# Optimization experiments

Measured on AMD Instinct MI355X. Metric: run time of the kernel, lower is better.

## Reference

```python
import jax, jax.numpy as jnp
import numpy as np

B, L, NS, D, M = 64, 200, 1000, 128, 50


def setup_inputs() -> dict:
    key = jax.random.key(0)
    ks = jax.random.split(key, 12)
    s = np.sqrt(2.0 / D).astype(np.float32)  # kaiming_normal scale for Mk/Mv0
    lw = np.sqrt(1.0 / D).astype(np.float32)
    return {
        "skills": jax.random.randint(ks[0], (B, L), 0, NS),
        "responses": jax.random.randint(ks[1], (B, L), 0, 2),
        "k_emb": jax.random.normal(ks[2], (NS, D), jnp.float32) * 0.02,
        "v_emb": jax.random.normal(ks[3], (2 * NS, D), jnp.float32) * 0.02,
        "Mk": jax.random.normal(ks[4], (M, D), jnp.float32) * s,
        "Mv0": jax.random.normal(ks[5], (M, D), jnp.float32) * s,
        "e_W": jax.random.normal(ks[6], (D, D), jnp.float32) * lw,
        "e_b": jnp.zeros((D,), jnp.float32),
        "a_W": jax.random.normal(ks[7], (D, D), jnp.float32) * lw,
        "a_b": jnp.zeros((D,), jnp.float32),
        "f_W": jax.random.normal(ks[8], (D, 2 * D), jnp.float32) * np.sqrt(1.0 / (2 * D)).astype(np.float32),
        "f_b": jnp.zeros((D,), jnp.float32),
        "p_W": jax.random.normal(ks[9], (1, D), jnp.float32) * lw,
        "p_b": jnp.zeros((1,), jnp.float32),
    }


def _dkvmn_forward(skills, responses, k_emb, v_emb, Mk, Mv0,
                   e_W, e_b, a_W, a_b, f_W, f_b, p_W, p_b):
    masked_r = responses * (responses > -1).astype(responses.dtype)
    x = skills + NS * masked_r                      # [B,L] combined (skill,response) id
    k = k_emb[skills]                               # [B,L,D]
    v = v_emb[x]                                    # [B,L,D]
    w = jax.nn.softmax(jnp.einsum('bld,md->blm', k, Mk), axis=-1)  # [B,L,M]
    e = jax.nn.sigmoid(v @ e_W.T + e_b)             # erase  [B,L,D]
    a = jnp.tanh(v @ a_W.T + a_b)                   # add    [B,L,D]

    def step(Mvt, wea):
        wt, et, at = wea                            # [B,M], [B,D], [B,D]
        u = wt[:, :, None]                          # [B,M,1]
        new = Mvt * (1.0 - u * et[:, None, :]) + u * at[:, None, :]
        return new, Mvt                             # emit PRE-update state (Mv[:, :-1])

    Mv_init = jnp.broadcast_to(Mv0[None], (B, M, D))
    _, Mv_pre = jax.lax.scan(
        step, Mv_init,
        (w.transpose(1, 0, 2), e.transpose(1, 0, 2), a.transpose(1, 0, 2)))
    # Mv_pre: [L,B,M,D]; weighted read of pre-update memory
    read = jnp.einsum('blm,lbmd->bld', w, Mv_pre)   # [B,L,D]
    f = jnp.tanh(jnp.concatenate([read, k], axis=-1) @ f_W.T + f_b)  # [B,L,D]
    p = jax.nn.sigmoid(f @ p_W.T + p_b)[..., 0]     # [B,L] (dropout off: eval)
    return p[:, 1:]                                 # pred, [B,L-1]


def reference(skills, responses, k_emb, v_emb, Mk, Mv0,
              e_W, e_b, a_W, a_b, f_W, f_b, p_W, p_b):
    return _dkvmn_forward(skills, responses, k_emb, v_emb, Mk, Mv0,
                          e_W, e_b, a_W, a_b, f_W, f_b, p_W, p_b)
```

## Files before the change

### kernel.cpp

```cpp
#include <hip/hip_runtime.h>
#include <hip/hip_bf16.h>

#define Bb 64
#define Ll 200
#define NSs 1000
#define Dd 128
#define Mm 50
#define CCk 8
#define TT 25

__device__ __forceinline__ float bcast_lane(float v, int l) {
    return __int_as_float(__builtin_amdgcn_readlane(__float_as_int(v), l));
}

__global__ void __launch_bounds__(256) kern_tab(
        const float* __restrict__ k_emb,
        const float* __restrict__ v_emb,
        const float* __restrict__ Mk,
        const float* __restrict__ e_W, const float* __restrict__ e_b,
        const float* __restrict__ a_W, const float* __restrict__ a_b,
        const float* __restrict__ f_W,
        float* __restrict__ wtab, float* __restrict__ etab,
        float* __restrict__ atab, float* __restrict__ fktab) {
    __shared__ float smem[12672];
    int tid = threadIdx.x;
    int wave = tid >> 6, lane = tid & 63;

    if (blockIdx.x >= 63 && blockIdx.x < 126) {
        int sk0 = (blockIdx.x - 63) * 16;
        float (*mk)[Dd + 4] = (float(*)[Dd + 4])smem;
        float (*kr)[Dd + 4] = (float(*)[Dd + 4])(smem + 6600);
        for (int lin = tid; lin < (Mm * Dd) / 4; lin += 256) {
            float4 f = ((const float4*)Mk)[lin];
            *(float4*)&mk[lin >> 5][(lin & 31) * 4] = f;
        }
        for (int lin = tid; lin < 16 * 32; lin += 256) {
            int r = lin >> 5, c4 = lin & 31;
            int sk = min(sk0 + r, NSs - 1);
            float4 f = ((const float4*)(k_emb + (size_t)sk * Dd))[c4];
            *(float4*)&kr[r][c4 * 4] = f;
        }
        __syncthreads();
        int mmr = (lane < Mm) ? lane : 0;
        float acc[4] = {0.f, 0.f, 0.f, 0.f};
#pragma unroll 2
        for (int q = 0; q < 32; ++q) {
            float4 mkv = *(const float4*)&mk[mmr][q * 4];
#pragma unroll
            for (int i = 0; i < 4; ++i) {
                float4 kv = *(const float4*)&kr[wave * 4 + i][q * 4];
                acc[i] = fmaf(mkv.x, kv.x, acc[i]);
                acc[i] = fmaf(mkv.y, kv.y, acc[i]);
                acc[i] = fmaf(mkv.z, kv.z, acc[i]);
                acc[i] = fmaf(mkv.w, kv.w, acc[i]);
            }
        }
#pragma unroll
        for (int i = 0; i < 4; ++i) {
            float logit = (lane < Mm) ? acc[i] : -1e30f;
            float mx = logit;
            for (int off = 32; off > 0; off >>= 1) mx = fmaxf(mx, __shfl_down(mx, off));
            mx = __shfl(mx, 0);
            float ex = (lane < Mm) ? expf(logit - mx) : 0.f;
            float sm = ex;
            for (int off = 32; off > 0; off >>= 1) sm += __shfl_down(sm, off);
            sm = __shfl(sm, 0);
            int sk = sk0 + wave * 4 + i;
            if (sk < NSs && lane < Mm) wtab[(size_t)sk * Mm + lane] = ex / sm;
        }
        return;
    }

    bool is_fk = (blockIdx.x >= 126);
    int r0 = is_fk ? (blockIdx.x - 126) * 32 : blockIdx.x * 32;
    int rmax = is_fk ? NSs : 2 * NSs;
    const float* src = is_fk ? k_emb : v_emb;

    float (*vt)[Dd + 4] = (float(*)[Dd + 4])smem;
    float (*wt)[Dd + 4] = (float(*)[Dd + 4])(smem + 4224);
#pragma unroll
    for (int i = 0; i < 4; ++i) {
        int lin = i * 256 + tid;
        int r = lin >> 5, c4 = lin & 31;
        int x = min(r0 + r, rmax - 1);
        float4 f = ((const float4*)(src + (size_t)x * Dd))[c4];
        *(float4*)&vt[r][c4 * 4] = f;
    }
    __syncthreads();
    int pg = lane >> 3, og = lane & 7;

    if (is_fk) {
        for (int sub = 0; sub < 2; ++sub) {
#pragma unroll
            for (int i = 0; i < 8; ++i) {
                int lin = i * 64 + lane;
                int r = lin >> 5, c4 = lin & 31;
                int row = wave * 32 + sub * 16 + r;
                float4 f = ((const float4*)(f_W + (size_t)row * (2 * Dd)))[32 + c4];
                *(float4*)&wt[wave * 16 + r][c4 * 4] = f;
            }
            float acc[4][2] = {};
#pragma unroll 2
            for (int q = 0; q < 32; ++q) {
                float4 av[4], bv[2];
#pragma unroll
                for (int i = 0; i < 4; ++i) av[i] = *(const float4*)&vt[pg + 8 * i][q * 4];
#pragma unroll
                for (int j = 0; j < 2; ++j) bv[j] = *(const float4*)&wt[wave * 16 + og + 8 * j][q * 4];
#pragma unroll
                for (int i = 0; i < 4; ++i)
#pragma unroll
                    for (int j = 0; j < 2; ++j) {
                        acc[i][j] = fmaf(av[i].x, bv[j].x, acc[i][j]);
                        acc[i][j] = fmaf(av[i].y, bv[j].y, acc[i][j]);
                        acc[i][j] = fmaf(av[i].z, bv[j].z, acc[i][j]);
                        acc[i][j] = fmaf(av[i].w, bv[j].w, acc[i][j]);
                    }
            }
#pragma unroll
            for (int j = 0; j < 2; ++j) {
                int row = wave * 32 + sub * 16 + og + 8 * j;
#pragma unroll
                for (int i = 0; i < 4; ++i) {
                    int sk = r0 + pg + 8 * i;
                    if (sk < NSs) fktab[(size_t)sk * Dd + row] = acc[i][j];
                }
            }
        }
    } else {
        for (int s = 0; s < 4; ++s) {
            int base_row = wave * 64 + s * 16;
            bool is_e = base_row < 128;
            const float* W = is_e ? e_W : a_W;
            int wrow0 = is_e ? base_row : base_row - 128;
#pragma unroll
            for (int i = 0; i < 8; ++i) {
                int lin = i * 64 + lane;
                int r = lin >> 5, c4 = lin & 31;
                float4 f = ((const float4*)(W + (size_t)(wrow0 + r) * Dd))[c4];
                *(float4*)&wt[wave * 16 + r][c4 * 4] = f;
            }
            float acc[4][2] = {};
#pragma unroll 2
            for (int q = 0; q < 32; ++q) {
                float4 av[4], bv[2];
#pragma unroll
                for (int i = 0; i < 4; ++i) av[i] = *(const float4*)&vt[pg + 8 * i][q * 4];
#pragma unroll
                for (int j = 0; j < 2; ++j) bv[j] = *(const float4*)&wt[wave * 16 + og + 8 * j][q * 4];
#pragma unroll
                for (int i = 0; i < 4; ++i)
#pragma unroll
                    for (int j = 0; j < 2; ++j) {
                        acc[i][j] = fmaf(av[i].x, bv[j].x, acc[i][j]);
                        acc[i][j] = fmaf(av[i].y, bv[j].y, acc[i][j]);
                        acc[i][j] = fmaf(av[i].z, bv[j].z, acc[i][j]);
                        acc[i][j] = fmaf(av[i].w, bv[j].w, acc[i][j]);
                    }
            }
            float* dst = is_e ? etab : atab;
#pragma unroll
            for (int j = 0; j < 2; ++j) {
                int row = wrow0 + og + 8 * j;
                float bias = (is_e ? e_b : a_b)[row];
#pragma unroll
                for (int i = 0; i < 4; ++i) {
                    int x = r0 + pg + 8 * i;
                    if (x < 2 * NSs) {
                        float v = acc[i][j] + bias;
                        dst[(size_t)x * Dd + row] = is_e ? (1.f / (1.f + expf(-v))) : tanhf(v);
                    }
                }
            }
        }
    }
}

#define TB_LOAD(S, tt) do { int _t = (tt);                                   \
    if (_t < TT) {                                                           \
        int _sk = __shfl(skv, _t);                                           \
        int _x  = __shfl(xv, _t);                                            \
        w##S = (lane < Mm) ? wtab[(size_t)_sk * Mm + lane] : 0.f;            \
        e##S = etab[(size_t)_x * Dd + d];                                    \
        a##S = atab[(size_t)_x * Dd + d]; } } while (0)

#define PQ_BODY(S) do {                                                      \
    _Pragma("unroll")                                                        \
    for (int m = 0; m < Mm; ++m) {                                           \
        float wm = bcast_lane(w##S, m);                                      \
        float A  = fmaf(-wm, e##S, 1.f);                                     \
        Q[m] = fmaf(A, Q[m], wm * a##S);                                     \
        P[m] *= A; } } while (0)

#define RD_BODY(S, tt) do {                                                  \
    float acc0 = 0.f, acc1 = 0.f;                                            \
    _Pragma("unroll")                                                        \
    for (int m = 0; m < Mm; m += 2) {                                        \
        float wm0 = bcast_lane(w##S, m);                                     \
        float wm1 = bcast_lane(w##S, m + 1);                                 \
        acc0 = fmaf(wm0, mv[m], acc0);                                       \
        mv[m] = fmaf(wm0, fmaf(-e##S, mv[m], a##S), mv[m]);                  \
        acc1 = fmaf(wm1, mv[m + 1], acc1);                                   \
        mv[m + 1] = fmaf(wm1, fmaf(-e##S, mv[m + 1], a##S), mv[m + 1]);      \
    }                                                                        \
    read_ws[(blBase + (tt)) * Dd + d] = acc0 + acc1;                         \
    } while (0)

__global__ void __launch_bounds__(128) kern_scan_pq(
        const int* __restrict__ skills,
        const int* __restrict__ responses,
        const float* __restrict__ wtab,
        const float* __restrict__ etab,
        const float* __restrict__ atab,
        float* __restrict__ P_ws, float* __restrict__ Q_ws) {
    int b = blockIdx.x / (CCk - 1), c = blockIdx.x % (CCk - 1);
    int d = threadIdx.x;
    int lane = d & 63;
    size_t blBase = (size_t)b * Ll + (size_t)c * TT;

    int skv = 0, xv = 0;
    if (lane < TT) {
        skv = skills[blBase + lane];
        int rr = responses[blBase + lane];
        xv = skv + NSs * ((rr > -1) ? rr : 0);
    }

    float P[Mm], Q[Mm];
#pragma unroll
    for (int m = 0; m < Mm; ++m) { P[m] = 1.f; Q[m] = 0.f; }

    float w0 = 0.f, e0 = 0.f, a0 = 0.f;
    float w1 = 0.f, e1 = 0.f, a1 = 0.f;
    float w2 = 0.f, e2 = 0.f, a2 = 0.f;
    TB_LOAD(0, 0);
    TB_LOAD(1, 1);
    for (int tt = 0; tt < TT; tt += 3) {
        TB_LOAD(2, tt + 2);  PQ_BODY(0);
        if (tt + 1 < TT) { TB_LOAD(0, tt + 3);  PQ_BODY(1); }
        if (tt + 2 < TT) { TB_LOAD(1, tt + 4);  PQ_BODY(2); }
    }
    size_t base = ((size_t)(b * (CCk - 1) + c)) * (Mm * Dd) + d;
#pragma unroll
    for (int m = 0; m < Mm; ++m) {
        P_ws[base + m * Dd] = P[m];
        Q_ws[base + m * Dd] = Q[m];
    }
}

__global__ void __launch_bounds__(128) kern_scan_rd(
        const int* __restrict__ skills,
        const int* __restrict__ responses,
        const float* __restrict__ Mv0,
        const float* __restrict__ wtab,
        const float* __restrict__ etab,
        const float* __restrict__ atab,
        const float* __restrict__ P_ws, const float* __restrict__ Q_ws,
        float* __restrict__ read_ws) {
    int b = blockIdx.x / CCk, c = blockIdx.x % CCk;
    int d = threadIdx.x;
    int lane = d & 63;
    size_t blBase = (size_t)b * Ll + (size_t)c * TT;

    int skv = 0, xv = 0;
    if (lane < TT) {
        skv = skills[blBase + lane];
        int rr = responses[blBase + lane];
        xv = skv + NSs * ((rr > -1) ? rr : 0);
    }

    float mv[Mm];
#pragma unroll
    for (int m = 0; m < Mm; ++m) mv[m] = Mv0[m * Dd + d];
    for (int cc = 0; cc < c; ++cc) {
        size_t base = ((size_t)(b * (CCk - 1) + cc)) * (Mm * Dd) + d;
#pragma unroll
        for (int m = 0; m < Mm; ++m)
            mv[m] = fmaf(P_ws[base + m * Dd], mv[m], Q_ws[base + m * Dd]);
    }

    float w0 = 0.f, e0 = 0.f, a0 = 0.f;
    float w1 = 0.f, e1 = 0.f, a1 = 0.f;
    float w2 = 0.f, e2 = 0.f, a2 = 0.f;
    TB_LOAD(0, 0);
    TB_LOAD(1, 1);
    for (int tt = 0; tt < TT; tt += 3) {
        TB_LOAD(2, tt + 2);  RD_BODY(0, tt);
        if (tt + 1 < TT) { TB_LOAD(0, tt + 3);  RD_BODY(1, tt + 1); }
        if (tt + 2 < TT) { TB_LOAD(1, tt + 4);  RD_BODY(2, tt + 2); }
    }
}

__global__ void __launch_bounds__(256) kern_out(
        const int* __restrict__ skills,
        const float* __restrict__ read_ws,
        const float* __restrict__ fktab,
        const float* __restrict__ f_W, const float* __restrict__ f_b,
        const float* __restrict__ p_W, const float* __restrict__ p_b,
        float* __restrict__ out) {
    __shared__ float ct[32][Dd + 4];
    __shared__ float fkt[32][Dd + 4];
    __shared__ float wt[4][16][Dd + 4];
    __shared__ float pf[32][8];
    int tid = threadIdx.x;
    int blk = blockIdx.x;

#pragma unroll
    for (int i = 0; i < 4; ++i) {
        int lin = i * 256 + tid;
        int r = lin >> 5, c4 = lin & 31;
        int idx = blk * 32 + r;
        int b = idx / (Ll - 1);
        int l = idx % (Ll - 1) + 1;
        int bl = b * Ll + l;
        float4 f = ((const float4*)(read_ws + (size_t)bl * Dd))[c4];
        *(float4*)&ct[r][c4 * 4] = f;
        int sk = skills[bl];
        float4 g = ((const float4*)(fktab + (size_t)sk * Dd))[c4];
        *(float4*)&fkt[r][c4 * 4] = g;
    }
    ((float*)pf)[tid] = 0.f;
    __syncthreads();

    int wave = tid >> 6, lane = tid & 63;
    int pg = lane >> 3, og = lane & 7;

    float ppart[4] = {0.f, 0.f, 0.f, 0.f};
    for (int sub = 0; sub < 2; ++sub) {
        float acc[4][2] = {};
#pragma unroll
        for (int i = 0; i < 8; ++i) {
            int lin = i * 64 + lane;
            int r = lin >> 5, c4 = lin & 31;
            int row = wave * 32 + sub * 16 + r;
            float4 f = ((const float4*)(f_W + (size_t)row * (2 * Dd)))[c4];
            *(float4*)&wt[wave][r][c4 * 4] = f;
        }
#pragma unroll 2
        for (int q = 0; q < 32; ++q) {
            float4 av[4], bv[2];
#pragma unroll
            for (int i = 0; i < 4; ++i) av[i] = *(const float4*)&ct[pg + 8 * i][q * 4];
#pragma unroll
            for (int j = 0; j < 2; ++j) bv[j] = *(const float4*)&wt[wave][og + 8 * j][q * 4];
#pragma unroll
            for (int i = 0; i < 4; ++i)
#pragma unroll
                for (int j = 0; j < 2; ++j) {
                    acc[i][j] = fmaf(av[i].x, bv[j].x, acc[i][j]);
                    acc[i][j] = fmaf(av[i].y, bv[j].y, acc[i][j]);
                    acc[i][j] = fmaf(av[i].z, bv[j].z, acc[i][j]);
                    acc[i][j] = fmaf(av[i].w, bv[j].w, acc[i][j]);
                }
        }
#pragma unroll
        for (int j = 0; j < 2; ++j) {
            int row = wave * 32 + sub * 16 + og + 8 * j;
            float fb = f_b[row];
            float pw = p_W[row];
#pragma unroll
            for (int i = 0; i < 4; ++i) {
                float fkv = fkt[pg + 8 * i][row];
                ppart[i] = fmaf(tanhf(acc[i][j] + fkv + fb), pw, ppart[i]);
            }
        }
    }
#pragma unroll
    for (int i = 0; i < 4; ++i) {
        float v = ppart[i];
        for (int off = 4; off > 0; off >>= 1) v += __shfl_down(v, off, 8);
        if (og == 0) pf[pg + 8 * i][wave] = v;
    }
    __syncthreads();
    if (tid < 32) {
        float s = pf[tid][0] + pf[tid][1] + pf[tid][2] + pf[tid][3] + p_b[0];
        out[blk * 32 + tid] = 1.f / (1.f + expf(-s));
    }
}

extern "C" void kernel_launch(void* const* d_in, const int* in_sizes, int n_in,
                              void* d_out, int out_size, void* d_ws, size_t ws_size,
                              hipStream_t stream) {
    const int*   skills    = (const int*)  d_in[0];
    const int*   responses = (const int*)  d_in[1];
    const float* k_emb     = (const float*)d_in[2];
    const float* v_emb     = (const float*)d_in[3];
    const float* Mk        = (const float*)d_in[4];
    const float* Mv0       = (const float*)d_in[5];
    const float* e_W       = (const float*)d_in[6];
    const float* e_b       = (const float*)d_in[7];
    const float* a_W       = (const float*)d_in[8];
    const float* a_b       = (const float*)d_in[9];
    const float* f_W       = (const float*)d_in[10];
    const float* f_b       = (const float*)d_in[11];
    const float* p_W       = (const float*)d_in[12];
    const float* p_b       = (const float*)d_in[13];
    (void)in_sizes; (void)n_in; (void)out_size; (void)ws_size;

    float* out = (float*)d_out;

    const size_t BLD = (size_t)Bb * Ll * Dd;
    const size_t BMD = (size_t)Bb * Mm * Dd;

    float* ws      = (float*)d_ws;
    float* read_ws = ws;
    float* P_ws    = read_ws + BLD;
    float* Q_ws    = P_ws + (CCk - 1) * BMD;
    float* wtab    = Q_ws + (CCk - 1) * BMD;
    float* etab    = wtab + (size_t)NSs * Mm;
    float* atab    = etab + (size_t)2 * NSs * Dd;
    float* fktab   = atab + (size_t)2 * NSs * Dd;

    kern_tab<<<158, 256, 0, stream>>>(k_emb, v_emb, Mk, e_W, e_b, a_W, a_b, f_W,
                                      wtab, etab, atab, fktab);
    kern_scan_pq<<<Bb * (CCk - 1), 128, 0, stream>>>(skills, responses,
                                                     wtab, etab, atab, P_ws, Q_ws);
    kern_scan_rd<<<Bb * CCk, 128, 0, stream>>>(skills, responses, Mv0,
                                               wtab, etab, atab, P_ws, Q_ws, read_ws);
    kern_out<<<Bb * (Ll - 1) / 32, 256, 0, stream>>>(skills, read_ws, fktab,
                                                     f_W, f_b, p_W, p_b, out);
}
```

Before: 181.3 us.

## Fuse scan read pass with output projection into one kernel

Merges the read-scan kernel and the output MLP kernel so the per-chunk read vectors stay in shared memory instead of round-tripping through a global workspace. Two waves run the scan while the other two stage the f_W tile and key features in parallel, then all four waves compute the projection for the chunk's 25 positions. This removes one launch and the read_ws traffic. In exchange each block reloads the 128x128 weight tile, uses a large shared-memory footprint that may limit occupancy, and wastes lanes on padded positions (25 of 32 rows).

```diff
diff --git a/kernel.cpp b/kernel.cpp
--- a/kernel.cpp
+++ b/kernel.cpp
@@ -203,7 +203,7 @@
         acc1 = fmaf(wm1, mv[m + 1], acc1);                                   \
         mv[m + 1] = fmaf(wm1, fmaf(-e##S, mv[m + 1], a##S), mv[m + 1]);      \
     }                                                                        \
-    read_ws[(blBase + (tt)) * Dd + d] = acc0 + acc1;                         \
+    rt[(tt)][d] = acc0 + acc1;                                               \
     } while (0)
 
 __global__ void __launch_bounds__(128) kern_scan_pq(
@@ -247,7 +247,7 @@
     }
 }
 
-__global__ void __launch_bounds__(128) kern_scan_rd(
+__global__ void __launch_bounds__(256) kern_rd_out(
         const int* __restrict__ skills,
         const int* __restrict__ responses,
         const float* __restrict__ Mv0,
@@ -255,113 +255,100 @@
         const float* __restrict__ etab,
         const float* __restrict__ atab,
         const float* __restrict__ P_ws, const float* __restrict__ Q_ws,
-        float* __restrict__ read_ws) {
-    int b = blockIdx.x / CCk, c = blockIdx.x % CCk;
-    int d = threadIdx.x;
-    int lane = d & 63;
-    size_t blBase = (size_t)b * Ll + (size_t)c * TT;
-
-    int skv = 0, xv = 0;
-    if (lane < TT) {
-        skv = skills[blBase + lane];
-        int rr = responses[blBase + lane];
-        xv = skv + NSs * ((rr > -1) ? rr : 0);
-    }
-
-    float mv[Mm];
-#pragma unroll
-    for (int m = 0; m < Mm; ++m) mv[m] = Mv0[m * Dd + d];
-    for (int cc = 0; cc < c; ++cc) {
-        size_t base = ((size_t)(b * (CCk - 1) + cc)) * (Mm * Dd) + d;
-#pragma unroll
-        for (int m = 0; m < Mm; ++m)
-            mv[m] = fmaf(P_ws[base + m * Dd], mv[m], Q_ws[base + m * Dd]);
-    }
-
-    float w0 = 0.f, e0 = 0.f, a0 = 0.f;
-    float w1 = 0.f, e1 = 0.f, a1 = 0.f;
-    float w2 = 0.f, e2 = 0.f, a2 = 0.f;
-    TB_LOAD(0, 0);
-    TB_LOAD(1, 1);
-    for (int tt = 0; tt < TT; tt += 3) {
-        TB_LOAD(2, tt + 2);  RD_BODY(0, tt);
-        if (tt + 1 < TT) { TB_LOAD(0, tt + 3);  RD_BODY(1, tt + 1); }
-        if (tt + 2 < TT) { TB_LOAD(1, tt + 4);  RD_BODY(2, tt + 2); }
-    }
-}
-
-__global__ void __launch_bounds__(256) kern_out(
-        const int* __restrict__ skills,
-        const float* __restrict__ read_ws,
         const float* __restrict__ fktab,
         const float* __restrict__ f_W, const float* __restrict__ f_b,
         const float* __restrict__ p_W, const float* __restrict__ p_b,
         float* __restrict__ out) {
-    __shared__ float ct[32][Dd + 4];
-    __shared__ float fkt[32][Dd + 4];
-    __shared__ float wt[4][16][Dd + 4];
-    __shared__ float pf[32][8];
+    __shared__ float wtile[Dd][Dd + 4];
+    __shared__ float rt[TT][Dd + 4];
+    __shared__ float fkt[TT][Dd + 4];
+    __shared__ float pf[32][4];
     int tid = threadIdx.x;
-    int blk = blockIdx.x;
-
-#pragma unroll
-    for (int i = 0; i < 4; ++i) {
-        int lin = i * 256 + tid;
-        int r = lin >> 5, c4 = lin & 31;
-        int idx = blk * 32 + r;
-        int b = idx / (Ll - 1);
-        int l = idx % (Ll - 1) + 1;
-        int bl = b * Ll + l;
-        float4 f = ((const float4*)(read_ws + (size_t)bl * Dd))[c4];
-        *(float4*)&ct[r][c4 * 4] = f;
-        int sk = skills[bl];
-        float4 g = ((const float4*)(fktab + (size_t)sk * Dd))[c4];
-        *(float4*)&fkt[r][c4 * 4] = g;
-    }
-    ((float*)pf)[tid] = 0.f;
+    int b = blockIdx.x / CCk, c = blockIdx.x % CCk;
+    size_t blBase = (size_t)b * Ll + (size_t)c * TT;
+
+    if (tid < 128) {
+        int d = tid;
+        int lane = d & 63;
+        int skv = 0, xv = 0;
+        if (lane < TT) {
+            skv = skills[blBase + lane];
+            int rr = responses[blBase + lane];
+            xv = skv + NSs * ((rr > -1) ? rr : 0);
+        }
+        float mv[Mm];
+#pragma unroll
+        for (int m = 0; m < Mm; ++m) mv[m] = Mv0[m * Dd + d];
+        for (int cc = 0; cc < c; ++cc) {
+            size_t base = ((size_t)(b * (CCk - 1) + cc)) * (Mm * Dd) + d;
+#pragma unroll
+            for (int m = 0; m < Mm; ++m)
+                mv[m] = fmaf(P_ws[base + m * Dd], mv[m], Q_ws[base + m * Dd]);
+        }
+        float w0 = 0.f, e0 = 0.f, a0 = 0.f;
+        float w1 = 0.f, e1 = 0.f, a1 = 0.f;
+        float w2 = 0.f, e2 = 0.f, a2 = 0.f;
+        TB_LOAD(0, 0);
+        TB_LOAD(1, 1);
+        for (int tt = 0; tt < TT; tt += 3) {
+            TB_LOAD(2, tt + 2);  RD_BODY(0, tt);
+            if (tt + 1 < TT) { TB_LOAD(0, tt + 3);  RD_BODY(1, tt + 1); }
+            if (tt + 2 < TT) { TB_LOAD(1, tt + 4);  RD_BODY(2, tt + 2); }
+        }
+    } else {
+        int u = tid - 128;
+#pragma unroll
+        for (int i = 0; i < 32; ++i) {
+            int lin = i * 128 + u;
+            int r = lin >> 5, c4 = lin & 31;
+            float4 f = ((const float4*)(f_W + (size_t)r * (2 * Dd)))[c4];
+            *(float4*)&wtile[r][c4 * 4] = f;
+        }
+        for (int lin = u; lin < TT * 32; lin += 128) {
+            int r = lin >> 5, c4 = lin & 31;
+            int sk = skills[blBase + r];
+            float4 f = ((const float4*)(fktab + (size_t)sk * Dd))[c4];
+            *(float4*)&fkt[r][c4 * 4] = f;
+        }
+    }
     __syncthreads();
 
     int wave = tid >> 6, lane = tid & 63;
     int pg = lane >> 3, og = lane & 7;
 
+    float acc[4][4] = {};
+#pragma unroll 2
+    for (int q = 0; q < 32; ++q) {
+        float4 av[4], bv[4];
+#pragma unroll
+        for (int i = 0; i < 4; ++i) {
+            int pos = pg + 8 * i;
+            av[i] = *(const float4*)&rt[(pos < TT) ? pos : 0][q * 4];
+        }
+#pragma unroll
+        for (int j = 0; j < 4; ++j) bv[j] = *(const float4*)&wtile[wave * 32 + og + 8 * j][q * 4];
+#pragma unroll
+        for (int i = 0; i < 4; ++i)
+#pragma unroll
+            for (int j = 0; j < 4; ++j) {
+                acc[i][j] = fmaf(av[i].x, bv[j].x, acc[i][j]);
+                acc[i][j] = fmaf(av[i].y, bv[j].y, acc[i][j]);
+                acc[i][j] = fmaf(av[i].z, bv[j].z, acc[i][j]);
+                acc[i][j] = fmaf(av[i].w, bv[j].w, acc[i][j]);
+            }
+    }
+
     float ppart[4] = {0.f, 0.f, 0.f, 0.f};
-    for (int sub = 0; sub < 2; ++sub) {
-        float acc[4][2] = {};
-#pragma unroll
-        for (int i = 0; i < 8; ++i) {
-            int lin = i * 64 + lane;
-            int r = lin >> 5, c4 = lin & 31;
-            int row = wave * 32 + sub * 16 + r;
-            float4 f = ((const float4*)(f_W + (size_t)row * (2 * Dd)))[c4];
-            *(float4*)&wt[wave][r][c4 * 4] = f;
-        }
-#pragma unroll 2
-        for (int q = 0; q < 32; ++q) {
-            float4 av[4], bv[2];
-#pragma unroll
-            for (int i = 0; i < 4; ++i) av[i] = *(const float4*)&ct[pg + 8 * i][q * 4];
-#pragma unroll
-            for (int j = 0; j < 2; ++j) bv[j] = *(const float4*)&wt[wave][og + 8 * j][q * 4];
-#pragma unroll
-            for (int i = 0; i < 4; ++i)
-#pragma unroll
-                for (int j = 0; j < 2; ++j) {
-                    acc[i][j] = fmaf(av[i].x, bv[j].x, acc[i][j]);
-                    acc[i][j] = fmaf(av[i].y, bv[j].y, acc[i][j]);
-                    acc[i][j] = fmaf(av[i].z, bv[j].z, acc[i][j]);
-                    acc[i][j] = fmaf(av[i].w, bv[j].w, acc[i][j]);
-                }
-        }
-#pragma unroll
-        for (int j = 0; j < 2; ++j) {
-            int row = wave * 32 + sub * 16 + og + 8 * j;
-            float fb = f_b[row];
-            float pw = p_W[row];
-#pragma unroll
-            for (int i = 0; i < 4; ++i) {
-                float fkv = fkt[pg + 8 * i][row];
-                ppart[i] = fmaf(tanhf(acc[i][j] + fkv + fb), pw, ppart[i]);
-            }
+#pragma unroll
+    for (int j = 0; j < 4; ++j) {
+        int row = wave * 32 + og + 8 * j;
+        float fb = f_b[row];
+        float pw = p_W[row];
+#pragma unroll
+        for (int i = 0; i < 4; ++i) {
+            int pos = pg + 8 * i;
+            float fkv = fkt[(pos < TT) ? pos : 0][row];
+            ppart[i] = fmaf(tanhf(acc[i][j] + fkv + fb), pw, ppart[i]);
         }
     }
 #pragma unroll
@@ -371,9 +358,12 @@
         if (og == 0) pf[pg + 8 * i][wave] = v;
     }
     __syncthreads();
-    if (tid < 32) {
-        float s = pf[tid][0] + pf[tid][1] + pf[tid][2] + pf[tid][3] + p_b[0];
-        out[blk * 32 + tid] = 1.f / (1.f + expf(-s));
+    if (tid < 32 && tid < TT) {
+        int l = c * TT + tid;
+        if (l >= 1) {
+            float s = pf[tid][0] + pf[tid][1] + pf[tid][2] + pf[tid][3] + p_b[0];
+            out[b * (Ll - 1) + (l - 1)] = 1.f / (1.f + expf(-s));
+        }
     }
 }
 
@@ -398,12 +388,10 @@
 
     float* out = (float*)d_out;
 
-    const size_t BLD = (size_t)Bb * Ll * Dd;
     const size_t BMD = (size_t)Bb * Mm * Dd;
 
     float* ws      = (float*)d_ws;
-    float* read_ws = ws;
-    float* P_ws    = read_ws + BLD;
+    float* P_ws    = ws;
     float* Q_ws    = P_ws + (CCk - 1) * BMD;
     float* wtab    = Q_ws + (CCk - 1) * BMD;
     float* etab    = wtab + (size_t)NSs * Mm;
@@ -414,8 +402,7 @@
                                       wtab, etab, atab, fktab);
     kern_scan_pq<<<Bb * (CCk - 1), 128, 0, stream>>>(skills, responses,
                                                      wtab, etab, atab, P_ws, Q_ws);
-    kern_scan_rd<<<Bb * CCk, 128, 0, stream>>>(skills, responses, Mv0,
-                                               wtab, etab, atab, P_ws, Q_ws, read_ws);
-    kern_out<<<Bb * (Ll - 1) / 32, 256, 0, stream>>>(skills, read_ws, fktab,
-                                                     f_W, f_b, p_W, p_b, out);
+    kern_rd_out<<<Bb * CCk, 256, 0, stream>>>(skills, responses, Mv0,
+                                              wtab, etab, atab, P_ws, Q_ws,
+                                              fktab, f_W, f_b, p_W, p_b, out);
 }
```

Measured after the change: 192.6 us. 1.06x slower.

## Add chunk-prefix combine kernel and split scan into more shorter chunks

Applied to the files above, without the earlier changes.

A new kernel combines the per-chunk affine (P,Q) transforms sequentially per memory element and stores each chunk's starting state. The read kernel then loads its starting state directly instead of replaying all earlier chunks' transforms, which removes work that grew with chunk index. Chunk count rises from 8 to 20, so each chunk is 10 steps long and more blocks run in parallel. The cost is an extra launch and more P/Q/S workspace traffic.

```diff
diff --git a/kernel.cpp b/kernel.cpp
--- a/kernel.cpp
+++ b/kernel.cpp
@@ -6,8 +6,8 @@
 #define NSs 1000
 #define Dd 128
 #define Mm 50
-#define CCk 8
-#define TT 25
+#define CCk 20
+#define TT 10
 
 __device__ __forceinline__ float bcast_lane(float v, int l) {
     return __int_as_float(__builtin_amdgcn_readlane(__float_as_int(v), l));
@@ -247,6 +247,28 @@
     }
 }
 
+__global__ void kern_scan_comb(
+        const float* __restrict__ Mv0,
+        const float* __restrict__ P_ws, const float* __restrict__ Q_ws,
+        float* __restrict__ S_ws) {
+    int idx = blockIdx.x * 256 + threadIdx.x;
+    int b   = idx / (Mm * Dd);
+    int md  = idx % (Mm * Dd);
+    float Pr[CCk - 1], Qr[CCk - 1];
+#pragma unroll
+    for (int c = 0; c < CCk - 1; ++c) {
+        size_t pq = ((size_t)(b * (CCk - 1) + c)) * (Mm * Dd) + md;
+        Pr[c] = P_ws[pq];
+        Qr[c] = Q_ws[pq];
+    }
+    float s = Mv0[md];
+#pragma unroll
+    for (int c = 0; c < CCk - 1; ++c) {
+        s = fmaf(Pr[c], s, Qr[c]);
+        S_ws[((size_t)(b * (CCk - 1) + c)) * (Mm * Dd) + md] = s;
+    }
+}
+
 __global__ void __launch_bounds__(128) kern_scan_rd(
         const int* __restrict__ skills,
         const int* __restrict__ responses,
@@ -254,7 +276,7 @@
         const float* __restrict__ wtab,
         const float* __restrict__ etab,
         const float* __restrict__ atab,
-        const float* __restrict__ P_ws, const float* __restrict__ Q_ws,
+        const float* __restrict__ S_ws,
         float* __restrict__ read_ws) {
     int b = blockIdx.x / CCk, c = blockIdx.x % CCk;
     int d = threadIdx.x;
@@ -269,13 +291,13 @@
     }
 
     float mv[Mm];
-#pragma unroll
-    for (int m = 0; m < Mm; ++m) mv[m] = Mv0[m * Dd + d];
-    for (int cc = 0; cc < c; ++cc) {
-        size_t base = ((size_t)(b * (CCk - 1) + cc)) * (Mm * Dd) + d;
-#pragma unroll
-        for (int m = 0; m < Mm; ++m)
-            mv[m] = fmaf(P_ws[base + m * Dd], mv[m], Q_ws[base + m * Dd]);
+    if (c == 0) {
+#pragma unroll
+        for (int m = 0; m < Mm; ++m) mv[m] = Mv0[m * Dd + d];
+    } else {
+        size_t sb = ((size_t)(b * (CCk - 1) + (c - 1))) * (Mm * Dd) + d;
+#pragma unroll
+        for (int m = 0; m < Mm; ++m) mv[m] = S_ws[sb + m * Dd];
     }
 
     float w0 = 0.f, e0 = 0.f, a0 = 0.f;
@@ -405,7 +427,8 @@
     float* read_ws = ws;
     float* P_ws    = read_ws + BLD;
     float* Q_ws    = P_ws + (CCk - 1) * BMD;
-    float* wtab    = Q_ws + (CCk - 1) * BMD;
+    float* S_ws    = Q_ws + (CCk - 1) * BMD;
+    float* wtab    = S_ws + (CCk - 1) * BMD;
     float* etab    = wtab + (size_t)NSs * Mm;
     float* atab    = etab + (size_t)2 * NSs * Dd;
     float* fktab   = atab + (size_t)2 * NSs * Dd;
@@ -414,8 +437,9 @@
                                       wtab, etab, atab, fktab);
     kern_scan_pq<<<Bb * (CCk - 1), 128, 0, stream>>>(skills, responses,
                                                      wtab, etab, atab, P_ws, Q_ws);
+    kern_scan_comb<<<(int)(BMD / 256), 256, 0, stream>>>(Mv0, P_ws, Q_ws, S_ws);
     kern_scan_rd<<<Bb * CCk, 128, 0, stream>>>(skills, responses, Mv0,
-                                               wtab, etab, atab, P_ws, Q_ws, read_ws);
+                                               wtab, etab, atab, S_ws, read_ws);
     kern_out<<<Bb * (Ll - 1) / 32, 256, 0, stream>>>(skills, read_ws, fktab,
                                                      f_W, f_b, p_W, p_b, out);
 }
```

Measured after the change: 167.0 us. 1.09x faster.
